# Optimization experiments

Measured on AMD Instinct MI355X. Metric: run time of the kernel, lower is better.

Reference implementation:

```python
import jax, jax.numpy as jnp
import numpy as np

N_NODES = 100000


def gcn_conv(x, W, b, src, dst, n):
    # PyG GCNConv: linear transform, add self-loops, symmetric degree norm, scatter-add, bias
    h = x @ W                                      # [n, d_out]
    loop = jnp.arange(n, dtype=src.dtype)
    s = jnp.concatenate([src, loop])               # [E + n]
    d = jnp.concatenate([dst, loop])
    deg = jax.ops.segment_sum(jnp.ones_like(d, dtype=h.dtype), d, num_segments=n)
    dinv = jnp.where(deg > 0, jax.lax.rsqrt(deg), 0.0)
    norm = dinv[s] * dinv[d]                       # [E + n]
    msg = h[s] * norm[:, None]                     # gather + scale
    out = jax.ops.segment_sum(msg, d, num_segments=n)  # scatter-add over targets
    return out + b


def setup_inputs() -> dict:
    key = jax.random.key(0)
    ks = jax.random.split(key, 8)
    n, c_in, hid, c_out = N_NODES, 256, 128, 64
    x = jax.random.normal(ks[0], (n, c_in), dtype=jnp.float32)
    edge_index = jax.random.randint(ks[1], (2, 1600000), 0, n, dtype=jnp.int64)
    s = 0.1
    return {
        "x": x,
        "edge_index": edge_index,
        "W1": jax.random.normal(ks[2], (c_in, hid), dtype=jnp.float32) * s,
        "b1": jnp.zeros((hid,), dtype=jnp.float32),
        "Wmu": jax.random.normal(ks[3], (hid, c_out), dtype=jnp.float32) * s,
        "bmu": jnp.zeros((c_out,), dtype=jnp.float32),
        "Wlv": jax.random.normal(ks[4], (hid, c_out), dtype=jnp.float32) * s,
        "blv": jnp.zeros((c_out,), dtype=jnp.float32),
    }


def reference(x, edge_index, W1, b1, Wmu, bmu, Wlv, blv):
    n = x.shape[0]
    src, dst = edge_index[0], edge_index[1]
    h = jax.nn.relu(gcn_conv(x, W1, b1, src, dst, n))
    mu = gcn_conv(h, Wmu, bmu, src, dst, n)
    logvar = gcn_conv(h, Wlv, blv, src, dst, n)
    return mu, logvar
```

## Files before the change

### kernel.cpp

```cpp
#include <hip/hip_runtime.h>


#define C_IN  256
#define HID   128
#define C_OUT 64
#define NBUCK 1024
#define P1WGS 256

typedef __attribute__((ext_vector_type(8))) short bf16x8;
typedef __attribute__((ext_vector_type(4))) float f32x4;

__device__ inline unsigned short f2bf(float f) {
  unsigned u = __float_as_uint(f);
  unsigned r = u + 0x7FFF + ((u >> 16) & 1);
  return (unsigned short)(r >> 16);
}
__device__ inline float bflo(unsigned v) { return __uint_as_float(v << 16); }
__device__ inline float bfhi(unsigned v) { return __uint_as_float(v & 0xFFFF0000u); }

__global__ __launch_bounds__(256) void k_bin_count(const int* __restrict__ dst,
                                                   int* __restrict__ histmat, int E) {
  __shared__ int h[NBUCK];
  int tid = threadIdx.x;
  for (int i = tid; i < NBUCK; i += 256) h[i] = 0;
  __syncthreads();
  for (int e = blockIdx.x * 256 + tid; e < E; e += P1WGS * 256)
    atomicAdd(&h[dst[e] >> 7], 1);
  __syncthreads();
  for (int i = tid; i < NBUCK; i += 256)
    histmat[blockIdx.x * NBUCK + i] = h[i];
}

__global__ __launch_bounds__(256) void k_col_scan(int* __restrict__ histmat,
                                                  int* __restrict__ bucket_tot) {
  __shared__ int sh[P1WGS];
  int b = blockIdx.x;
  int t = threadIdx.x;
  int v = histmat[t * NBUCK + b];
  sh[t] = v; __syncthreads();
  for (int ofs = 1; ofs < P1WGS; ofs <<= 1) {
    int add = (t >= ofs) ? sh[t - ofs] : 0;
    __syncthreads();
    sh[t] += add;
    __syncthreads();
  }
  histmat[t * NBUCK + b] = sh[t] - v;
  if (t == P1WGS - 1) bucket_tot[b] = sh[t];
}

__global__ void k_bucket_scan(const int* __restrict__ bucket_tot,
                              int* __restrict__ bucket_start, int E) {
  __shared__ int sh[NBUCK];
  int t = threadIdx.x;
  int v = bucket_tot[t];
  sh[t] = v; __syncthreads();
  for (int ofs = 1; ofs < NBUCK; ofs <<= 1) {
    int add = (t >= ofs) ? sh[t - ofs] : 0;
    __syncthreads();
    sh[t] += add;
    __syncthreads();
  }
  bucket_start[t] = sh[t] - v;
  if (t == NBUCK - 1) bucket_start[NBUCK] = E;
}

__global__ __launch_bounds__(256) void k_bin_scatter(const int* __restrict__ src,
                                                     const int* __restrict__ dst,
                                                     const int* __restrict__ histmat,
                                                     const int* __restrict__ bucket_start,
                                                     unsigned* __restrict__ binned, int E) {
  __shared__ int cur[NBUCK];
  int tid = threadIdx.x;
  for (int i = tid; i < NBUCK; i += 256)
    cur[i] = bucket_start[i] + histmat[blockIdx.x * NBUCK + i];
  __syncthreads();
  for (int e = blockIdx.x * 256 + tid; e < E; e += P1WGS * 256) {
    int d = dst[e];
    int pos = atomicAdd(&cur[d >> 7], 1);
    binned[pos] = (unsigned)src[e] | ((unsigned)(d & 127) << 17);
  }
}

__global__ __launch_bounds__(256) void k_bucket_csr(const unsigned* __restrict__ binned,
                                                    const int* __restrict__ bucket_start,
                                                    int* __restrict__ row_start,
                                                    float* __restrict__ dinv,
                                                    int* __restrict__ csr_src,
                                                    int n, int E) {
  __shared__ int h[128], ls[128], c[128];
  int b = blockIdx.x, t = threadIdx.x;
  int start = bucket_start[b], end = bucket_start[b + 1];
  if (t < 128) h[t] = 0;
  __syncthreads();
  for (int e = start + t; e < end; e += 256)
    atomicAdd(&h[binned[e] >> 17], 1);
  __syncthreads();
  if (t < 128) ls[t] = h[t];
  __syncthreads();
  for (int ofs = 1; ofs < 128; ofs <<= 1) {
    int add = (t < 128 && t >= ofs) ? ls[t - ofs] : 0;
    __syncthreads();
    if (t < 128) ls[t] += add;
    __syncthreads();
  }
  if (t < 128) {
    int excl = ls[t] - h[t];
    ls[t] = excl;
    c[t] = excl;
    int node = b * 128 + t;
    if (node < n) {
      row_start[node] = start + excl;
      dinv[node] = rsqrtf((float)h[t] + 1.0f);
    }
  }
  if (b == 0 && t == 0) row_start[n] = E;
  __syncthreads();
  for (int e = start + t; e < end; e += 256) {
    unsigned v = binned[e];
    int pos = start + atomicAdd(&c[v >> 17], 1);
    csr_src[pos] = (int)(v & 0x1FFFF);
  }
}

__global__ void k_prep(const float* __restrict__ W1, const float* __restrict__ Wmu,
                       const float* __restrict__ Wlv,
                       unsigned short* __restrict__ bswz1,
                       unsigned short* __restrict__ bswz2,
                       unsigned* __restrict__ p1z, unsigned* __restrict__ p2z) {
  int idx = blockIdx.x * 256 + threadIdx.x;
  if (idx < 4096) {
    int L = idx & 63, t = (idx >> 6) & 7, s = idx >> 9;
    const float* srcp = W1 + (size_t)(s * 32 + ((L >> 4) << 3)) * 128 + t * 16 + (L & 15);
    unsigned short* dstp = bswz1 + (size_t)idx * 8;
#pragma unroll
    for (int j = 0; j < 8; j++) dstp[j] = f2bf(srcp[(size_t)j * 128]);
  } else if (idx < 6144) {
    int id2 = idx - 4096;
    int L = id2 & 63, t = (id2 >> 6) & 7, s = id2 >> 9;
    int nn = t * 16 + (L & 15);
    int k0 = s * 32 + ((L >> 4) << 3);
    const float* W = (nn < C_OUT) ? (Wmu + nn) : (Wlv + (nn - C_OUT));
    unsigned short* dstp = bswz2 + (size_t)id2 * 8;
#pragma unroll
    for (int j = 0; j < 8; j++) dstp[j] = f2bf(W[(size_t)(k0 + j) * C_OUT]);
  } else if (idx < 6208) {
    p1z[idx - 6144] = 0u;
  } else if (idx < 6272) {
    p2z[idx - 6208] = 0u;
  }
}

template <typename AT, int K>
__global__ __launch_bounds__(256) void k_gemm_mfma(const AT* __restrict__ A,
                                                   const unsigned short* __restrict__ bswz,
                                                   unsigned short* __restrict__ C,
                                                   const float* __restrict__ dinv,
                                                   int M) {
  constexpr int NS = K / 32;
  int wave = threadIdx.x >> 6, lane = threadIdx.x & 63;
  int m0 = blockIdx.x * 64 + wave * 16;
  int lrow = lane & 15, lq = lane >> 4;
  int arow = m0 + lrow;
  bool rv = arow < M;
  const AT* ap = A + (size_t)(rv ? arow : 0) * K + lq * 8;

  auto loadA = [&](int s) -> bf16x8 {
    if (sizeof(AT) == 4) {
      const float* af = (const float*)ap + s * 32;
      float4 u0 = rv ? *(const float4*)(af) : float4{0, 0, 0, 0};
      float4 u1 = rv ? *(const float4*)(af + 4) : float4{0, 0, 0, 0};
      union { unsigned short us[8]; bf16x8 v; } tmp;
      tmp.us[0] = f2bf(u0.x); tmp.us[1] = f2bf(u0.y);
      tmp.us[2] = f2bf(u0.z); tmp.us[3] = f2bf(u0.w);
      tmp.us[4] = f2bf(u1.x); tmp.us[5] = f2bf(u1.y);
      tmp.us[6] = f2bf(u1.z); tmp.us[7] = f2bf(u1.w);
      return tmp.v;
    } else {
      const unsigned short* ab = (const unsigned short*)ap + s * 32;
      return rv ? *(const bf16x8*)(ab) : (bf16x8)(short)0;
    }
  };

  f32x4 acc[8];
#pragma unroll
  for (int t = 0; t < 8; t++) acc[t] = (f32x4){0.f, 0.f, 0.f, 0.f};

  bf16x8 a_cur = loadA(0);
  bf16x8 b_cur[8];
#pragma unroll
  for (int t = 0; t < 8; t++)
    b_cur[t] = *(const bf16x8*)(bswz + lane * 8 + t * 512);

#pragma unroll
  for (int s = 0; s < NS; ++s) {
    bf16x8 a_nxt = a_cur;
    bf16x8 b_nxt[8];
    if (s + 1 < NS) {
      a_nxt = loadA(s + 1);
      const unsigned short* bp = bswz + (size_t)(s + 1) * 4096 + lane * 8;
#pragma unroll
      for (int t = 0; t < 8; t++) b_nxt[t] = *(const bf16x8*)(bp + t * 512);
    }
#pragma unroll
    for (int t = 0; t < 8; t++)
      acc[t] = __builtin_amdgcn_mfma_f32_16x16x32_bf16(a_cur, b_cur[t], acc[t], 0, 0, 0);
    a_cur = a_nxt;
    if (s + 1 < NS) {
#pragma unroll
      for (int t = 0; t < 8; t++) b_cur[t] = b_nxt[t];
    }
  }
#pragma unroll
  for (int i = 0; i < 4; i++) {
    int rr = m0 + lq * 4 + i;
    if (rr < M) {
      float dsc = dinv[rr];
      unsigned short* cp = C + (size_t)rr * 128 + lrow;
#pragma unroll
      for (int t = 0; t < 8; t++) cp[t * 16] = f2bf(acc[t][i] * dsc);
    }
  }
}

#define AGG_V4_BODY                                                                 \
  int tid = threadIdx.x;                                                            \
  int wid4 = blockIdx.x * 4 + (tid >> 6);                  \
  int lane = tid & 63;                                                              \
  int li = lane & 15;                                                               \
  int node = (wid4 << 2) + (lane >> 4);                                             \
  int rs = 0, re = -1;                                                              \
  if (node < n) { rs = row_start[node]; re = row_start[node + 1]; }                 \
  int mc = re - rs + 1;                                       \
  mc = max(mc, __shfl_xor(mc, 16, 64));                                             \
  mc = max(mc, __shfl_xor(mc, 32, 64));                                             \
  int maxcnt = __builtin_amdgcn_readfirstlane(mc);                                  \
  const char* pb = (const char*)p;                                                  \
  unsigned loff = (unsigned)(li << 4);                                              \
  int vb = (lane & 48) << 2;          \
  float acc[8];                                                                     \
  _Pragma("unroll")                                                                 \
  for (int j = 0; j < 8; ++j) acc[j] = 0.f;                                         \
  for (int t0 = 0; t0 < maxcnt; t0 += 16) {                                         \
    int s = rs + t0 + li;                                                           \
    int sl = n;                                                       \
    if (s < re) sl = csr[s];                                                        \
    else if (s == re) sl = node;                                     \
    int km = maxcnt - t0; if (km > 16) km = 16;                                     \
    for (int k = 0; k < km; k += 4) {                                               \
      int sk0 = __builtin_amdgcn_ds_bpermute(vb + ((k + 0) << 2), sl);              \
      int sk1 = __builtin_amdgcn_ds_bpermute(vb + ((k + 1) << 2), sl);              \
      int sk2 = __builtin_amdgcn_ds_bpermute(vb + ((k + 2) << 2), sl);              \
      int sk3 = __builtin_amdgcn_ds_bpermute(vb + ((k + 3) << 2), sl);              \
      uint4 v0 = *(const uint4*)(pb + ((((unsigned)sk0) << 8) + loff));             \
      uint4 v1 = *(const uint4*)(pb + ((((unsigned)sk1) << 8) + loff));             \
      uint4 v2 = *(const uint4*)(pb + ((((unsigned)sk2) << 8) + loff));             \
      uint4 v3 = *(const uint4*)(pb + ((((unsigned)sk3) << 8) + loff));             \
      acc[0] += bflo(v0.x); acc[1] += bfhi(v0.x);                                   \
      acc[2] += bflo(v0.y); acc[3] += bfhi(v0.y);                                   \
      acc[4] += bflo(v0.z); acc[5] += bfhi(v0.z);                                   \
      acc[6] += bflo(v0.w); acc[7] += bfhi(v0.w);                                   \
      acc[0] += bflo(v1.x); acc[1] += bfhi(v1.x);                                   \
      acc[2] += bflo(v1.y); acc[3] += bfhi(v1.y);                                   \
      acc[4] += bflo(v1.z); acc[5] += bfhi(v1.z);                                   \
      acc[6] += bflo(v1.w); acc[7] += bfhi(v1.w);                                   \
      acc[0] += bflo(v2.x); acc[1] += bfhi(v2.x);                                   \
      acc[2] += bflo(v2.y); acc[3] += bfhi(v2.y);                                   \
      acc[4] += bflo(v2.z); acc[5] += bfhi(v2.z);                                   \
      acc[6] += bflo(v2.w); acc[7] += bfhi(v2.w);                                   \
      acc[0] += bflo(v3.x); acc[1] += bfhi(v3.x);                                   \
      acc[2] += bflo(v3.y); acc[3] += bfhi(v3.y);                                   \
      acc[4] += bflo(v3.z); acc[5] += bfhi(v3.z);                                   \
      acc[6] += bflo(v3.w); acc[7] += bfhi(v3.w);                                   \
    }                                                                               \
  }

__global__ __launch_bounds__(256) void k_agg_relu_bf(
    const unsigned short* __restrict__ p, const float* __restrict__ dinv,
    const int* __restrict__ row_start, const int* __restrict__ csr,
    const float* __restrict__ bias, unsigned short* __restrict__ h, int n) {
  AGG_V4_BODY
  if (node < n) {
    float di = dinv[node];
    float4 ba = *(const float4*)(bias + (li << 3));
    float4 bb = *(const float4*)(bias + (li << 3) + 4);
    float r0 = fmaxf(acc[0] * di + ba.x, 0.f);
    float r1 = fmaxf(acc[1] * di + ba.y, 0.f);
    float r2 = fmaxf(acc[2] * di + ba.z, 0.f);
    float r3 = fmaxf(acc[3] * di + ba.w, 0.f);
    float r4 = fmaxf(acc[4] * di + bb.x, 0.f);
    float r5 = fmaxf(acc[5] * di + bb.y, 0.f);
    float r6 = fmaxf(acc[6] * di + bb.z, 0.f);
    float r7 = fmaxf(acc[7] * di + bb.w, 0.f);
    uint4 u;
    u.x = (unsigned)f2bf(r0) | ((unsigned)f2bf(r1) << 16);
    u.y = (unsigned)f2bf(r2) | ((unsigned)f2bf(r3) << 16);
    u.z = (unsigned)f2bf(r4) | ((unsigned)f2bf(r5) << 16);
    u.w = (unsigned)f2bf(r6) | ((unsigned)f2bf(r7) << 16);
    *(uint4*)((char*)h + (((size_t)node) << 8) + loff) = u;
  }
}

__global__ __launch_bounds__(256) void k_agg_out_bf(
    const unsigned short* __restrict__ p, const float* __restrict__ dinv,
    const int* __restrict__ row_start, const int* __restrict__ csr,
    const float* __restrict__ bmu, const float* __restrict__ blv,
    float* __restrict__ out, int n) {
  AGG_V4_BODY
  if (node < n) {
    float di = dinv[node];
    const float* bp = (li < 8) ? (bmu + (li << 3)) : (blv + ((li - 8) << 3));
    float* op = (li < 8) ? (out + (size_t)node * C_OUT + (li << 3))
                         : (out + (size_t)(n + node) * C_OUT + ((li - 8) << 3));
    float4 b0 = *(const float4*)(bp);
    float4 b1 = *(const float4*)(bp + 4);
    float4 o0 = {acc[0] * di + b0.x, acc[1] * di + b0.y,
                 acc[2] * di + b0.z, acc[3] * di + b0.w};
    float4 o1 = {acc[4] * di + b1.x, acc[5] * di + b1.y,
                 acc[6] * di + b1.z, acc[7] * di + b1.w};
    *(float4*)op = o0;
    *(float4*)(op + 4) = o1;
  }
}

extern "C" void kernel_launch(void* const* d_in, const int* in_sizes, int n_in,
                              void* d_out, int out_size, void* d_ws, size_t ws_size,
                              hipStream_t stream) {
  const float* x   = (const float*)d_in[0];
  const int*   ei  = (const int*)d_in[1];
  const float* W1  = (const float*)d_in[2];
  const float* b1  = (const float*)d_in[3];
  const float* Wmu = (const float*)d_in[4];
  const float* bmu = (const float*)d_in[5];
  const float* Wlv = (const float*)d_in[6];
  const float* blv = (const float*)d_in[7];
  float* out = (float*)d_out;

  const int n = in_sizes[0] / C_IN;
  const int E = in_sizes[1] / 2;
  const int* src = ei;
  const int* dst = ei + E;

  char* w = (char*)d_ws;
  auto alloc = [&](size_t bytes) -> void* {
    void* pp = (void*)w;
    w += (bytes + 255) & ~(size_t)255;
    return pp;
  };
  float*          dinv       = (float*)alloc((size_t)n * 4);
  int*            row_start  = (int*)alloc((size_t)(n + 1) * 4);
  int*            histmat    = (int*)alloc((size_t)P1WGS * NBUCK * 4);
  int*            bucket_tot = (int*)alloc((size_t)NBUCK * 4);
  int*            bucket_st  = (int*)alloc((size_t)(NBUCK + 1) * 4);
  unsigned*       binned     = (unsigned*)alloc((size_t)E * 4);
  int*            csr_src    = (int*)alloc((size_t)E * 4);
  unsigned short* bswz1      = (unsigned short*)alloc((size_t)C_IN * 128 * 2);
  unsigned short* bswz2      = (unsigned short*)alloc((size_t)HID * 128 * 2);
  unsigned short* p1         = (unsigned short*)alloc((size_t)(n + 1) * 128 * 2);
  unsigned short* hbuf       = (unsigned short*)alloc((size_t)n * 128 * 2);
  unsigned short* p2         = (unsigned short*)alloc((size_t)(n + 1) * 128 * 2);
  (void)ws_size; (void)n_in; (void)out_size;

  const int TB = 256;
  const int gemm_bks = (n + 63) / 64;
  const int agg_bks = (n + 15) / 16;
  const int nbk_csr = (n + 127) / 128;

  k_bin_count<<<P1WGS, TB, 0, stream>>>(dst, histmat, E);
  k_col_scan<<<NBUCK, TB, 0, stream>>>(histmat, bucket_tot);
  k_bucket_scan<<<1, NBUCK, 0, stream>>>(bucket_tot, bucket_st, E);
  k_bin_scatter<<<P1WGS, TB, 0, stream>>>(src, dst, histmat, bucket_st, binned, E);
  k_bucket_csr<<<nbk_csr, TB, 0, stream>>>(binned, bucket_st, row_start, dinv,
                                           csr_src, n, E);

  k_prep<<<25, 256, 0, stream>>>(W1, Wmu, Wlv, bswz1, bswz2,
                                 (unsigned*)(p1 + (size_t)n * 128),
                                 (unsigned*)(p2 + (size_t)n * 128));

  k_gemm_mfma<float, C_IN><<<gemm_bks, TB, 0, stream>>>(x, bswz1, p1, dinv, n);
  k_agg_relu_bf<<<agg_bks, TB, 0, stream>>>(p1, dinv, row_start, csr_src, b1, hbuf, n);

  k_gemm_mfma<unsigned short, HID><<<gemm_bks, TB, 0, stream>>>(hbuf, bswz2, p2, dinv, n);
  k_agg_out_bf<<<agg_bks, TB, 0, stream>>>(p2, dinv, row_start, csr_src, bmu, blv, out, n);
}
```

Before: 404.3 us.

## Sort CSR rows and gather half-rows in two passes with 8 lanes per node

Adds a per-row insertion-sort kernel so each node's source indices are in ascending order, which should improve locality of the feature gathers. The aggregation kernels are restructured to map 8 lanes per node, with 8 nodes per wave, and to gather each 256-byte row in two 128-byte halves. Each half pass touches a smaller footprint, with the aim of better cache behaviour and fewer wasted lanes on short rows. The trade-off is an extra kernel launch, serial per-thread sorting, and reloading the CSR indices on the second pass.

```diff
diff --git a/kernel.cpp b/kernel.cpp
--- a/kernel.cpp
+++ b/kernel.cpp
@@ -119,6 +119,19 @@
     unsigned v = binned[e];
     int pos = start + atomicAdd(&c[v >> 17], 1);
     csr_src[pos] = (int)(v & 0x1FFFF);
+  }
+}
+
+__global__ __launch_bounds__(256) void k_row_sort(const int* __restrict__ row_start,
+                                                  int* __restrict__ csr, int n) {
+  int i = blockIdx.x * 256 + threadIdx.x;
+  if (i >= n) return;
+  int rs = row_start[i], re = row_start[i + 1];
+  for (int a = rs + 1; a < re; ++a) {
+    int v = csr[a];
+    int b = a - 1;
+    while (b >= rs && csr[b] > v) { csr[b + 1] = csr[b]; --b; }
+    csr[b + 1] = v;
   }
 }
 
@@ -222,81 +235,93 @@
   }
 }
 
-#define AGG_V4_BODY                                                                 \
+__device__ __forceinline__ void gather_half(const char* pb,
+                                            const int* __restrict__ csr,
+                                            int n, int node, int rs, int re,
+                                            int maxcnt, int li, int vb,
+                                            unsigned hoff, float acc[8]) {
+#pragma unroll
+  for (int j = 0; j < 8; ++j) acc[j] = 0.f;
+  for (int t0 = 0; t0 < maxcnt; t0 += 8) {
+    int s = rs + t0 + li;
+    int sl = n;
+    if (s < re) sl = csr[s];
+    else if (s == re) sl = node;
+    int km = maxcnt - t0; if (km > 8) km = 8;
+    for (int k = 0; k < km; k += 4) {
+      int sk0 = __builtin_amdgcn_ds_bpermute(vb + ((k + 0) << 2), sl);
+      int sk1 = __builtin_amdgcn_ds_bpermute(vb + ((k + 1) << 2), sl);
+      int sk2 = __builtin_amdgcn_ds_bpermute(vb + ((k + 2) << 2), sl);
+      int sk3 = __builtin_amdgcn_ds_bpermute(vb + ((k + 3) << 2), sl);
+      uint4 v0 = *(const uint4*)(pb + ((((unsigned)sk0) << 8) + hoff));
+      uint4 v1 = *(const uint4*)(pb + ((((unsigned)sk1) << 8) + hoff));
+      uint4 v2 = *(const uint4*)(pb + ((((unsigned)sk2) << 8) + hoff));
+      uint4 v3 = *(const uint4*)(pb + ((((unsigned)sk3) << 8) + hoff));
+      acc[0] += bflo(v0.x); acc[1] += bfhi(v0.x);
+      acc[2] += bflo(v0.y); acc[3] += bfhi(v0.y);
+      acc[4] += bflo(v0.z); acc[5] += bfhi(v0.z);
+      acc[6] += bflo(v0.w); acc[7] += bfhi(v0.w);
+      acc[0] += bflo(v1.x); acc[1] += bfhi(v1.x);
+      acc[2] += bflo(v1.y); acc[3] += bfhi(v1.y);
+      acc[4] += bflo(v1.z); acc[5] += bfhi(v1.z);
+      acc[6] += bflo(v1.w); acc[7] += bfhi(v1.w);
+      acc[0] += bflo(v2.x); acc[1] += bfhi(v2.x);
+      acc[2] += bflo(v2.y); acc[3] += bfhi(v2.y);
+      acc[4] += bflo(v2.z); acc[5] += bfhi(v2.z);
+      acc[6] += bflo(v2.w); acc[7] += bfhi(v2.w);
+      acc[0] += bflo(v3.x); acc[1] += bfhi(v3.x);
+      acc[2] += bflo(v3.y); acc[3] += bfhi(v3.y);
+      acc[4] += bflo(v3.z); acc[5] += bfhi(v3.z);
+      acc[6] += bflo(v3.w); acc[7] += bfhi(v3.w);
+    }
+  }
+}
+
+#define AGG8_SETUP                                                                  \
   int tid = threadIdx.x;                                                            \
-  int wid4 = blockIdx.x * 4 + (tid >> 6);                  \
+  int wv = blockIdx.x * 4 + (tid >> 6);                             \
   int lane = tid & 63;                                                              \
-  int li = lane & 15;                                                               \
-  int node = (wid4 << 2) + (lane >> 4);                                             \
+  int li = lane & 7;                                                                \
+  int node = (wv << 3) + (lane >> 3);                             \
   int rs = 0, re = -1;                                                              \
   if (node < n) { rs = row_start[node]; re = row_start[node + 1]; }                 \
   int mc = re - rs + 1;                                       \
+  mc = max(mc, __shfl_xor(mc, 8, 64));                                              \
   mc = max(mc, __shfl_xor(mc, 16, 64));                                             \
   mc = max(mc, __shfl_xor(mc, 32, 64));                                             \
   int maxcnt = __builtin_amdgcn_readfirstlane(mc);                                  \
   const char* pb = (const char*)p;                                                  \
-  unsigned loff = (unsigned)(li << 4);                                              \
-  int vb = (lane & 48) << 2;          \
-  float acc[8];                                                                     \
-  _Pragma("unroll")                                                                 \
-  for (int j = 0; j < 8; ++j) acc[j] = 0.f;                                         \
-  for (int t0 = 0; t0 < maxcnt; t0 += 16) {                                         \
-    int s = rs + t0 + li;                                                           \
-    int sl = n;                                                       \
-    if (s < re) sl = csr[s];                                                        \
-    else if (s == re) sl = node;                                     \
-    int km = maxcnt - t0; if (km > 16) km = 16;                                     \
-    for (int k = 0; k < km; k += 4) {                                               \
-      int sk0 = __builtin_amdgcn_ds_bpermute(vb + ((k + 0) << 2), sl);              \
-      int sk1 = __builtin_amdgcn_ds_bpermute(vb + ((k + 1) << 2), sl);              \
-      int sk2 = __builtin_amdgcn_ds_bpermute(vb + ((k + 2) << 2), sl);              \
-      int sk3 = __builtin_amdgcn_ds_bpermute(vb + ((k + 3) << 2), sl);              \
-      uint4 v0 = *(const uint4*)(pb + ((((unsigned)sk0) << 8) + loff));             \
-      uint4 v1 = *(const uint4*)(pb + ((((unsigned)sk1) << 8) + loff));             \
-      uint4 v2 = *(const uint4*)(pb + ((((unsigned)sk2) << 8) + loff));             \
-      uint4 v3 = *(const uint4*)(pb + ((((unsigned)sk3) << 8) + loff));             \
-      acc[0] += bflo(v0.x); acc[1] += bfhi(v0.x);                                   \
-      acc[2] += bflo(v0.y); acc[3] += bfhi(v0.y);                                   \
-      acc[4] += bflo(v0.z); acc[5] += bfhi(v0.z);                                   \
-      acc[6] += bflo(v0.w); acc[7] += bfhi(v0.w);                                   \
-      acc[0] += bflo(v1.x); acc[1] += bfhi(v1.x);                                   \
-      acc[2] += bflo(v1.y); acc[3] += bfhi(v1.y);                                   \
-      acc[4] += bflo(v1.z); acc[5] += bfhi(v1.z);                                   \
-      acc[6] += bflo(v1.w); acc[7] += bfhi(v1.w);                                   \
-      acc[0] += bflo(v2.x); acc[1] += bfhi(v2.x);                                   \
-      acc[2] += bflo(v2.y); acc[3] += bfhi(v2.y);                                   \
-      acc[4] += bflo(v2.z); acc[5] += bfhi(v2.z);                                   \
-      acc[6] += bflo(v2.w); acc[7] += bfhi(v2.w);                                   \
-      acc[0] += bflo(v3.x); acc[1] += bfhi(v3.x);                                   \
-      acc[2] += bflo(v3.y); acc[3] += bfhi(v3.y);                                   \
-      acc[4] += bflo(v3.z); acc[5] += bfhi(v3.z);                                   \
-      acc[6] += bflo(v3.w); acc[7] += bfhi(v3.w);                                   \
-    }                                                                               \
-  }
+  int vb = (lane & 56) << 2;
 
 __global__ __launch_bounds__(256) void k_agg_relu_bf(
     const unsigned short* __restrict__ p, const float* __restrict__ dinv,
     const int* __restrict__ row_start, const int* __restrict__ csr,
     const float* __restrict__ bias, unsigned short* __restrict__ h, int n) {
-  AGG_V4_BODY
-  if (node < n) {
-    float di = dinv[node];
-    float4 ba = *(const float4*)(bias + (li << 3));
-    float4 bb = *(const float4*)(bias + (li << 3) + 4);
-    float r0 = fmaxf(acc[0] * di + ba.x, 0.f);
-    float r1 = fmaxf(acc[1] * di + ba.y, 0.f);
-    float r2 = fmaxf(acc[2] * di + ba.z, 0.f);
-    float r3 = fmaxf(acc[3] * di + ba.w, 0.f);
-    float r4 = fmaxf(acc[4] * di + bb.x, 0.f);
-    float r5 = fmaxf(acc[5] * di + bb.y, 0.f);
-    float r6 = fmaxf(acc[6] * di + bb.z, 0.f);
-    float r7 = fmaxf(acc[7] * di + bb.w, 0.f);
-    uint4 u;
-    u.x = (unsigned)f2bf(r0) | ((unsigned)f2bf(r1) << 16);
-    u.y = (unsigned)f2bf(r2) | ((unsigned)f2bf(r3) << 16);
-    u.z = (unsigned)f2bf(r4) | ((unsigned)f2bf(r5) << 16);
-    u.w = (unsigned)f2bf(r6) | ((unsigned)f2bf(r7) << 16);
-    *(uint4*)((char*)h + (((size_t)node) << 8) + loff) = u;
+  AGG8_SETUP
+  float di = (node < n) ? dinv[node] : 0.f;
+  for (int pass = 0; pass < 2; ++pass) {
+    float acc[8];
+    gather_half(pb, csr, n, node, rs, re, maxcnt, li, vb,
+                (unsigned)(pass * 128 + li * 16), acc);
+    if (node < n) {
+      const float* bb = bias + pass * 64 + (li << 3);
+      float4 b0 = *(const float4*)bb;
+      float4 b1 = *(const float4*)(bb + 4);
+      float r0 = fmaxf(acc[0] * di + b0.x, 0.f);
+      float r1 = fmaxf(acc[1] * di + b0.y, 0.f);
+      float r2 = fmaxf(acc[2] * di + b0.z, 0.f);
+      float r3 = fmaxf(acc[3] * di + b0.w, 0.f);
+      float r4 = fmaxf(acc[4] * di + b1.x, 0.f);
+      float r5 = fmaxf(acc[5] * di + b1.y, 0.f);
+      float r6 = fmaxf(acc[6] * di + b1.z, 0.f);
+      float r7 = fmaxf(acc[7] * di + b1.w, 0.f);
+      uint4 u;
+      u.x = (unsigned)f2bf(r0) | ((unsigned)f2bf(r1) << 16);
+      u.y = (unsigned)f2bf(r2) | ((unsigned)f2bf(r3) << 16);
+      u.z = (unsigned)f2bf(r4) | ((unsigned)f2bf(r5) << 16);
+      u.w = (unsigned)f2bf(r6) | ((unsigned)f2bf(r7) << 16);
+      *(uint4*)((char*)h + (((size_t)node) << 8) + (unsigned)(pass * 128 + li * 16)) = u;
+    }
   }
 }
 
@@ -305,20 +330,24 @@
     const int* __restrict__ row_start, const int* __restrict__ csr,
     const float* __restrict__ bmu, const float* __restrict__ blv,
     float* __restrict__ out, int n) {
-  AGG_V4_BODY
-  if (node < n) {
-    float di = dinv[node];
-    const float* bp = (li < 8) ? (bmu + (li << 3)) : (blv + ((li - 8) << 3));
-    float* op = (li < 8) ? (out + (size_t)node * C_OUT + (li << 3))
-                         : (out + (size_t)(n + node) * C_OUT + ((li - 8) << 3));
-    float4 b0 = *(const float4*)(bp);
-    float4 b1 = *(const float4*)(bp + 4);
-    float4 o0 = {acc[0] * di + b0.x, acc[1] * di + b0.y,
-                 acc[2] * di + b0.z, acc[3] * di + b0.w};
-    float4 o1 = {acc[4] * di + b1.x, acc[5] * di + b1.y,
-                 acc[6] * di + b1.z, acc[7] * di + b1.w};
-    *(float4*)op = o0;
-    *(float4*)(op + 4) = o1;
+  AGG8_SETUP
+  float di = (node < n) ? dinv[node] : 0.f;
+  for (int pass = 0; pass < 2; ++pass) {
+    float acc[8];
+    gather_half(pb, csr, n, node, rs, re, maxcnt, li, vb,
+                (unsigned)(pass * 128 + li * 16), acc);
+    if (node < n) {
+      const float* bp = (pass == 0 ? bmu : blv) + (li << 3);
+      float* op = out + ((size_t)(pass ? (n + node) : node)) * C_OUT + (li << 3);
+      float4 b0 = *(const float4*)bp;
+      float4 b1 = *(const float4*)(bp + 4);
+      float4 o0 = {acc[0] * di + b0.x, acc[1] * di + b0.y,
+                   acc[2] * di + b0.z, acc[3] * di + b0.w};
+      float4 o1 = {acc[4] * di + b1.x, acc[5] * di + b1.y,
+                   acc[6] * di + b1.z, acc[7] * di + b1.w};
+      *(float4*)op = o0;
+      *(float4*)(op + 4) = o1;
+    }
   }
 }
 
@@ -362,8 +391,9 @@
 
   const int TB = 256;
   const int gemm_bks = (n + 63) / 64;
-  const int agg_bks = (n + 15) / 16;
+  const int agg_bks = (n + 31) / 32;
   const int nbk_csr = (n + 127) / 128;
+  const int sort_bks = (n + 255) / 256;
 
   k_bin_count<<<P1WGS, TB, 0, stream>>>(dst, histmat, E);
   k_col_scan<<<NBUCK, TB, 0, stream>>>(histmat, bucket_tot);
@@ -371,6 +401,7 @@
   k_bin_scatter<<<P1WGS, TB, 0, stream>>>(src, dst, histmat, bucket_st, binned, E);
   k_bucket_csr<<<nbk_csr, TB, 0, stream>>>(binned, bucket_st, row_start, dinv,
                                            csr_src, n, E);
+  k_row_sort<<<sort_bks, TB, 0, stream>>>(row_start, csr_src, n);
 
   k_prep<<<25, 256, 0, stream>>>(W1, Wmu, Wlv, bswz1, bswz2,
                                  (unsigned*)(p1 + (size_t)n * 128),
```

After: 500.9 us. 1.24x slower.
